# Kernel tuning notes

Measured on AMD Instinct MI355X. Metric: run time of the kernel, lower is better.

The kernel has to match this reference:

```python
import jax, jax.numpy as jnp
import numpy as np
import math

B, S, D, H = 4, 2048, 1024, 16
DK = D // H  # 64
THETA = 10000.0


def setup_inputs() -> dict:
    key = jax.random.key(0)
    ks = jax.random.split(key, 5)
    std = 0.02
    return {
        "x": jax.random.normal(ks[0], (B, S, D), dtype=jnp.float32),
        "Wq": jax.random.normal(ks[1], (D, D), dtype=jnp.float32) * std,
        "Wk": jax.random.normal(ks[2], (D, D), dtype=jnp.float32) * std,
        "Wv": jax.random.normal(ks[3], (D, D), dtype=jnp.float32) * std,
        "Wo": jax.random.normal(ks[4], (D, D), dtype=jnp.float32) * std / math.sqrt(2 * 12),
        "token_positions": jnp.arange(S, dtype=jnp.int32),
    }


def _rope(x, pos):
    # x: [B, H, S, DK]; pos: [S]. Interleaved-pair rotary embedding.
    inv_freq = THETA ** (-jnp.arange(0, DK, 2, dtype=jnp.float32) / DK)  # [DK/2]
    ang = pos.astype(jnp.float32)[:, None] * inv_freq[None, :]  # [S, DK/2]
    cos, sin = jnp.cos(ang), jnp.sin(ang)
    x1, x2 = x[..., 0::2], x[..., 1::2]  # [B, H, S, DK/2]
    r1 = x1 * cos - x2 * sin
    r2 = x1 * sin + x2 * cos
    return jnp.stack([r1, r2], axis=-1).reshape(x.shape)


def reference(x, Wq, Wk, Wv, Wo, token_positions):
    b, s, d = x.shape
    Q = x @ Wq
    K = x @ Wk
    V = x @ Wv
    # [B, S, D] -> [B, H, S, DK]
    def split(t):
        return t.reshape(b, s, H, DK).transpose(0, 2, 1, 3)
    Qh, Kh, Vh = split(Q), split(K), split(V)
    Qh = _rope(Qh, token_positions)
    Kh = _rope(Kh, token_positions)
    scores = jnp.einsum('bhqd,bhkd->bhqk', Qh, Kh) / math.sqrt(DK)
    causal = jnp.tril(jnp.ones((s, s), dtype=bool))
    scores = jnp.where(causal, scores, -jnp.inf)
    probs = jax.nn.softmax(scores, axis=-1)
    out = jnp.einsum('bhqk,bhkd->bhqd', probs, Vh)
    out = out.transpose(0, 2, 1, 3).reshape(b, s, d)
    return out @ Wo
```

## Files before the change

### kernel.cpp

```cpp
#include <hip/hip_runtime.h>
#include <hip/hip_bf16.h>

#define B_N 4
#define S_LEN 2048
#define D_MODEL 1024
#define N_HEAD 16
#define D_HEAD 64
#define M_ROWS (B_N * S_LEN)

typedef short bf16x8 __attribute__((ext_vector_type(8)));
typedef short bf16x4 __attribute__((ext_vector_type(4)));
typedef float f32x4 __attribute__((ext_vector_type(4)));

#if __has_builtin(__builtin_amdgcn_mfma_f32_16x16x16bf16_1k)
#define HAVE_MFMA16 1
#else
#define HAVE_MFMA16 0
#endif

__device__ __forceinline__ unsigned short f2bf(float f) {
  union { float f; unsigned int u; } v; v.f = f;
  unsigned int r = v.u + 0x7FFFu + ((v.u >> 16) & 1u);
  return (unsigned short)(r >> 16);
}
__device__ __forceinline__ float bf2f(unsigned short u) {
  union { unsigned int u; float f; } v; v.u = ((unsigned int)u) << 16;
  return v.f;
}
__device__ __forceinline__ unsigned int pkbf(float a, float b) {
  union { __hip_bfloat162 h; unsigned int u; } cv;
  cv.h = __float22bfloat162_rn(make_float2(a, b));
  return cv.u;
}
__device__ __forceinline__ bf16x8 ld8(const unsigned short* p) {
  return *reinterpret_cast<const bf16x8*>(p);
}
__device__ __forceinline__ bf16x4 ld4(const unsigned short* p) {
  return *reinterpret_cast<const bf16x4*>(p);
}
__device__ __forceinline__ void glds16(const unsigned short* g, unsigned short* l) {
  __builtin_amdgcn_global_load_lds(
      (const __attribute__((address_space(1))) unsigned int*)g,
      (__attribute__((address_space(3))) unsigned int*)l, 16, 0, 0);
}

__global__ __launch_bounds__(256) void rope_tab_k(const int* __restrict__ pos,
                                                  float2* __restrict__ tab) {
  const int idx = blockIdx.x * 256 + threadIdx.x;
  const int s = idx >> 5;
  const int i = idx & 31;
  const float inv = exp2f(-(float)i * 0.41524101186092029f);
  const float ang = (float)pos[s] * inv;
  tab[idx] = make_float2(cosf(ang), sinf(ang));
}

__global__ __launch_bounds__(256) void cast_k(const float* __restrict__ X,
                                              unsigned short* __restrict__ Y) {
  const size_t i = ((size_t)blockIdx.x * 256 + threadIdx.x) * 8;
  const float4 a = *reinterpret_cast<const float4*>(X + i);
  const float4 b = *reinterpret_cast<const float4*>(X + i + 4);
  union { unsigned int u[4]; uint4 v; } o;
  o.u[0] = pkbf(a.x, a.y); o.u[1] = pkbf(a.z, a.w);
  o.u[2] = pkbf(b.x, b.y); o.u[3] = pkbf(b.z, b.w);
  *reinterpret_cast<uint4*>(Y + i) = o.v;
}

__global__ __launch_bounds__(256) void wtrans_k(
    const float* __restrict__ W0, const float* __restrict__ W1,
    const float* __restrict__ W2, const float* __restrict__ W3,
    unsigned short* __restrict__ T0, unsigned short* __restrict__ T1,
    unsigned short* __restrict__ T2, unsigned short* __restrict__ T3) {
  const int z = blockIdx.z;
  const float* __restrict__ W = (z == 0) ? W0 : (z == 1) ? W1 : (z == 2) ? W2 : W3;
  unsigned short* __restrict__ T = (z == 0) ? T0 : (z == 1) ? T1 : (z == 2) ? T2 : T3;
  __shared__ __align__(16) unsigned short tile[64][72];
  const int kb = blockIdx.x * 64;
  const int nb = blockIdx.y * 64;
#pragma unroll
  for (int it = 0; it < 2; ++it) {
    const int chunk = it * 256 + threadIdx.x;
    const int r = chunk >> 3;
    const int c8 = (chunk & 7) * 8;
    const float* src = W + (size_t)(kb + r) * D_MODEL + nb + c8;
    const float4 a = *reinterpret_cast<const float4*>(src);
    const float4 b = *reinterpret_cast<const float4*>(src + 4);
    union { unsigned int u[4]; uint4 v; } o;
    o.u[0] = pkbf(a.x, a.y); o.u[1] = pkbf(a.z, a.w);
    o.u[2] = pkbf(b.x, b.y); o.u[3] = pkbf(b.z, b.w);
    *reinterpret_cast<uint4*>(&tile[r][c8]) = o.v;
  }
  __syncthreads();
#pragma unroll
  for (int it = 0; it < 2; ++it) {
    const int chunk = it * 256 + threadIdx.x;
    const int n = chunk >> 3;
    const int k8 = (chunk & 7) * 8;
    __align__(16) unsigned short vals[8];
#pragma unroll
    for (int j = 0; j < 8; ++j) vals[j] = tile[k8 + j][n];
    *reinterpret_cast<uint4*>(T + (size_t)(nb + n) * D_MODEL + kb + k8) =
        *reinterpret_cast<const uint4*>(vals);
  }
}

__global__ __launch_bounds__(512, 1) void gemm8_k(
    const unsigned short* __restrict__ A, const unsigned short* __restrict__ W,
    unsigned short* __restrict__ Qo, unsigned short* __restrict__ Ko,
    unsigned short* __restrict__ VTo, float* __restrict__ OF,
    const float2* __restrict__ tab) {
  __shared__ __align__(16) unsigned short smem[3][384 * 64];

  const int tid = threadIdx.x;
  const int lane = tid & 63;
  const int w = tid >> 6;
  const int l15 = lane & 15;
  const int l4 = lane >> 4;
  const int wm = w >> 2;
  const int wn = w & 3;

  const int row0 = blockIdx.x * 128;
  const int col0 = blockIdx.y * 256;

  const int srow = lane >> 3;
  const int schunk = (lane & 7) ^ srow;
  const unsigned short* gA = A + (size_t)(row0 + w * 8 + srow) * D_MODEL + schunk * 8;
  const unsigned short* gB = W + (size_t)(col0 + w * 8 + srow) * D_MODEL + schunk * 8;

  const int swz = l15 & 7;
  const int kc0 = ((l4) ^ swz) * 8;
  const int kc1 = ((l4 + 4) ^ swz) * 8;

  f32x4 acc[4][4];
  const f32x4 fz = {0.f, 0.f, 0.f, 0.f};
#pragma unroll
  for (int m = 0; m < 4; ++m)
#pragma unroll
    for (int n = 0; n < 4; ++n) acc[m][n] = fz;

#define G8_STAGE_A(SL, T)                                                      \
  do {                                                                         \
    unsigned short* sa_ = &smem[SL][(w * 8) * 64];                             \
    const unsigned short* g_ = gA + (size_t)(T) * 64;                          \
    glds16(g_, sa_);                                                           \
    glds16(g_ + 64 * D_MODEL, sa_ + 64 * 64);                                  \
  } while (0)

#define G8_STAGE_B(SL, T)                                                      \
  do {                                                                         \
    unsigned short* sb_ = &smem[SL][(128 + w * 8) * 64];                       \
    const unsigned short* g_ = gB + (size_t)(T) * 64;                          \
    glds16(g_, sb_);                                                           \
    glds16(g_ + 64 * D_MODEL, sb_ + 64 * 64);                                  \
    glds16(g_ + 128 * D_MODEL, sb_ + 128 * 64);                                \
    glds16(g_ + 192 * D_MODEL, sb_ + 192 * 64);                                \
  } while (0)

#define G8_PHASE(SL, KC, STG)                                                  \
  do {                                                                         \
    const unsigned short* As_ = &smem[SL][0];                                  \
    const unsigned short* Bs_ = &smem[SL][128 * 64];                           \
    bf16x8 af_[4], bf_[4];                                                     \
    _Pragma("unroll") for (int mi = 0; mi < 4; ++mi)                           \
      af_[mi] = ld8(As_ + (wm * 64 + mi * 16 + l15) * 64 + (KC));              \
    _Pragma("unroll") for (int ni = 0; ni < 4; ++ni)                           \
      bf_[ni] = ld8(Bs_ + (wn * 64 + ni * 16 + l15) * 64 + (KC));              \
    STG;                                                                       \
    __builtin_amdgcn_s_barrier();                                              \
    __builtin_amdgcn_s_setprio(1);                                             \
    _Pragma("unroll") for (int mi = 0; mi < 4; ++mi)                           \
      _Pragma("unroll") for (int ni = 0; ni < 4; ++ni)                         \
        acc[mi][ni] = __builtin_amdgcn_mfma_f32_16x16x32_bf16(                 \
            af_[mi], bf_[ni], acc[mi][ni], 0, 0, 0);                           \
    __builtin_amdgcn_s_setprio(0);                                             \
    __builtin_amdgcn_s_barrier();                                              \
  } while (0)

  G8_STAGE_A(0, 0); G8_STAGE_B(0, 0);
  G8_STAGE_A(1, 1); G8_STAGE_B(1, 1);

#pragma unroll
  for (int t = 0; t < 16; ++t) {
    const int sl = t % 3;
    const int sp = (t + 2) % 3;
    if (t < 15) {
      asm volatile("s_waitcnt vmcnt(6)" ::: "memory");
    } else {
      asm volatile("s_waitcnt vmcnt(0)" ::: "memory");
    }
    __builtin_amdgcn_s_barrier();
    if (t < 14) {
      G8_PHASE(sl, kc0, G8_STAGE_A(sp, (t + 2)));
      G8_PHASE(sl, kc1, G8_STAGE_B(sp, (t + 2)));
    } else {
      G8_PHASE(sl, kc0, ((void)0));
      G8_PHASE(sl, kc1, ((void)0));
    }
  }
#undef G8_STAGE_A
#undef G8_STAGE_B
#undef G8_PHASE

  if (OF) {
#pragma unroll
    for (int ni = 0; ni < 4; ++ni) {
      const int gcol = col0 + wn * 64 + ni * 16 + l15;
#pragma unroll
      for (int mi = 0; mi < 4; ++mi)
#pragma unroll
        for (int r = 0; r < 4; ++r)
          OF[(size_t)(row0 + wm * 64 + mi * 16 + l4 * 4 + r) * D_MODEL + gcol] =
              acc[mi][ni][r];
    }
    return;
  }

  unsigned short(*T)[68] =
      (unsigned short(*)[68])(&smem[0][0] + w * 4352);
  const int gcb = col0 + wn * 64;
  const bool isV = (gcb >= 2048);
  const int lr = lane >> 3;
  const int lc = lane & 7;

  if (!isV) {
#pragma unroll
    for (int mi = 0; mi < 4; ++mi)
#pragma unroll
      for (int n = 0; n < 4; ++n)
#pragma unroll
        for (int r = 0; r < 4; ++r)
          T[mi * 16 + l4 * 4 + r][n * 16 + l15] = f2bf(acc[mi][n][r]);
  } else {
#pragma unroll
    for (int mi = 0; mi < 4; ++mi)
#pragma unroll
      for (int n = 0; n < 4; ++n)
#pragma unroll
        for (int r = 0; r < 4; ++r)
          T[n * 16 + l15][mi * 16 + l4 * 4 + r] = f2bf(acc[mi][n][r]);
  }
  if (!isV) {
    const bool isQ = (gcb < 1024);
    unsigned short* O = isQ ? Qo : Ko;
    const float qs = isQ ? 0.18033688011112042f : 1.0f;
    const int cbase = gcb & 1023;
#pragma unroll
    for (int rg = 0; rg < 8; ++rg) {
      const int trow = rg * 8 + lr;
      const int grow = row0 + wm * 64 + trow;
      const int s = grow & (S_LEN - 1);
      const bf16x8 vv = ld8(&T[trow][lc * 8]);
      const float4 tA = *reinterpret_cast<const float4*>(&tab[s * 32 + lc * 4]);
      const float4 tB = *reinterpret_cast<const float4*>(&tab[s * 32 + lc * 4 + 2]);
      float x[8];
#pragma unroll
      for (int j = 0; j < 8; ++j) x[j] = bf2f((unsigned short)vv[j]);
      union { unsigned int u[4]; uint4 v; } o;
      o.u[0] = pkbf((x[0] * tA.x - x[1] * tA.y) * qs, (x[0] * tA.y + x[1] * tA.x) * qs);
      o.u[1] = pkbf((x[2] * tA.z - x[3] * tA.w) * qs, (x[2] * tA.w + x[3] * tA.z) * qs);
      o.u[2] = pkbf((x[4] * tB.x - x[5] * tB.y) * qs, (x[4] * tB.y + x[5] * tB.x) * qs);
      o.u[3] = pkbf((x[6] * tB.z - x[7] * tB.w) * qs, (x[6] * tB.w + x[7] * tB.z) * qs);
      *reinterpret_cast<uint4*>(O + (size_t)grow * D_MODEL + cbase + lc * 8) = o.v;
    }
  } else {
    const int vc0 = gcb - 2048;
    const int h = vc0 >> 6;
    const int bb = row0 >> 11;
    const int s0 = (row0 & (S_LEN - 1)) + wm * 64;
#pragma unroll
    for (int rg = 0; rg < 8; ++rg) {
      const int dk = rg * 8 + lr;
      const bf16x8 vv = ld8(&T[dk][lc * 8]);
      *reinterpret_cast<bf16x8*>(
          VTo + ((size_t)((bb << 4) + h) * 64 + dk) * S_LEN + s0 + lc * 8) = vv;
    }
  }
}

__global__ __launch_bounds__(512) void attn6_k(
    const unsigned short* __restrict__ Q, const unsigned short* __restrict__ K,
    const unsigned short* __restrict__ VT, unsigned short* __restrict__ O) {
  const int pair = blockIdx.x;
  const int h = blockIdx.y;
  const int b = blockIdx.z;
  const int tid = threadIdx.x;
  const int w = tid >> 6;
  const int lane = tid & 63;
  const int l15 = lane & 15;
  const int l4 = lane >> 4;

  __shared__ __align__(16) unsigned short Ks[64][72];
  __shared__ __align__(16) unsigned short Vs[64][72];
#if !HAVE_MFMA16
  __shared__ __align__(16) unsigned short Ps[8][16][72];
#endif

  const f32x4 fz = {0.f, 0.f, 0.f, 0.f};
  const unsigned short* kbase = K + (size_t)b * S_LEN * D_MODEL + h * D_HEAD;
  const unsigned short* vbase = VT + (size_t)((b << 4) + h) * 64 * S_LEN;

  const int rr = tid >> 3;
  const int c8 = (tid & 7) * 8;

  for (int half = 0; half < 2; ++half) {
    const int qt = half ? (15 - pair) : pair;
    const int qb = qt * 128;
    const int qw0 = qb + w * 16;

    bf16x8 qf[2];
#pragma unroll
    for (int kc = 0; kc < 2; ++kc)
      qf[kc] = ld8(Q + (size_t)(b * S_LEN + qw0 + l15) * D_MODEL +
                   h * D_HEAD + kc * 32 + l4 * 8);

    f32x4 o[4];
#pragma unroll
    for (int d = 0; d < 4; ++d) o[d] = fz;
    float lsum = 0.f;

    const int nkt = qb / 64 + 2;
    uint4 kreg = *reinterpret_cast<const uint4*>(kbase + (size_t)rr * D_MODEL + c8);
    uint4 vreg = *reinterpret_cast<const uint4*>(vbase + (size_t)rr * S_LEN + c8);

    for (int kt = 0; kt < nkt; ++kt) {
      const int kb0 = kt * 64;
      *reinterpret_cast<uint4*>(&Ks[rr][c8]) = kreg;
      *reinterpret_cast<uint4*>(&Vs[rr][c8]) = vreg;
      if (kt + 1 < nkt) {
        const int nb0 = kb0 + 64;
        kreg = *reinterpret_cast<const uint4*>(kbase + (size_t)(nb0 + rr) * D_MODEL + c8);
        vreg = *reinterpret_cast<const uint4*>(vbase + (size_t)rr * S_LEN + nb0 + c8);
      }
      __syncthreads();

      if (kb0 <= qw0 + 15) {
        f32x4 s[4];
#pragma unroll
        for (int n = 0; n < 4; ++n) {
          const bf16x8 kf0 = ld8(&Ks[n * 16 + l15][l4 * 8]);
          const bf16x8 kf1 = ld8(&Ks[n * 16 + l15][32 + l4 * 8]);
          f32x4 a0 = __builtin_amdgcn_mfma_f32_16x16x32_bf16(kf0, qf[0], fz, 0, 0, 0);
          s[n] = __builtin_amdgcn_mfma_f32_16x16x32_bf16(kf1, qf[1], a0, 0, 0, 0);
        }
        bf16x4 pf[4];
        const bool full = (kb0 + 63 <= qw0);
        const int q = qw0 + l15;
        float su = lsum;
#pragma unroll
        for (int n = 0; n < 4; ++n) {
          float e[4];
          if (full) {
#pragma unroll
            for (int r = 0; r < 4; ++r) e[r] = exp2f(s[n][r]);
          } else {
#pragma unroll
            for (int r = 0; r < 4; ++r) {
              const int key = kb0 + n * 16 + l4 * 4 + r;
              const float v = exp2f(s[n][r]);
              e[r] = (key <= q) ? v : 0.f;
            }
          }
          su += (e[0] + e[1]) + (e[2] + e[3]);
          union { unsigned int u[2]; bf16x4 v; } pk;
          pk.u[0] = pkbf(e[0], e[1]);
          pk.u[1] = pkbf(e[2], e[3]);
          pf[n] = pk.v;
        }
        lsum = su;

#if HAVE_MFMA16
#pragma unroll
        for (int d = 0; d < 4; ++d) {
          bf16x4 vfc[4];
#pragma unroll
          for (int c = 0; c < 4; ++c) vfc[c] = ld4(&Vs[d * 16 + l15][c * 16 + l4 * 4]);
#pragma unroll
          for (int c = 0; c < 4; ++c)
            o[d] = __builtin_amdgcn_mfma_f32_16x16x16bf16_1k(vfc[c], pf[c], o[d], 0, 0, 0);
        }
#else
#pragma unroll
        for (int n = 0; n < 4; ++n)
          *reinterpret_cast<bf16x4*>(&Ps[w][l15][n * 16 + l4 * 4]) = pf[n];
        bf16x8 pfr[2];
#pragma unroll
        for (int kc = 0; kc < 2; ++kc)
          pfr[kc] = ld8(&Ps[w][l15][kc * 32 + l4 * 8]);
#pragma unroll
        for (int d = 0; d < 4; ++d) {
          const bf16x8 vf0 = ld8(&Vs[d * 16 + l15][l4 * 8]);
          const bf16x8 vf1 = ld8(&Vs[d * 16 + l15][32 + l4 * 8]);
          o[d] = __builtin_amdgcn_mfma_f32_16x16x32_bf16(vf0, pfr[0], o[d], 0, 0, 0);
          o[d] = __builtin_amdgcn_mfma_f32_16x16x32_bf16(vf1, pfr[1], o[d], 0, 0, 0);
        }
#endif
      }
      __syncthreads();
    }

    float s = lsum;
    s += __shfl_xor(s, 16);
    s += __shfl_xor(s, 32);
    const float li = 1.0f / s;
    unsigned short* op = O + (size_t)(b * S_LEN + qw0 + l15) * D_MODEL +
                         h * D_HEAD + l4 * 4;
#pragma unroll
    for (int d = 0; d < 4; ++d) {
      union { unsigned int u[2]; uint2 v; } ov;
      ov.u[0] = pkbf(o[d][0] * li, o[d][1] * li);
      ov.u[1] = pkbf(o[d][2] * li, o[d][3] * li);
      *reinterpret_cast<uint2*>(op + d * 16) = ov.v;
    }
  }
}

extern "C" void kernel_launch(void* const* d_in, const int* in_sizes, int n_in,
                              void* d_out, int out_size, void* d_ws, size_t ws_size,
                              hipStream_t stream) {
  const float* x  = (const float*)d_in[0];
  const float* Wq = (const float*)d_in[1];
  const float* Wk = (const float*)d_in[2];
  const float* Wv = (const float*)d_in[3];
  const float* Wo = (const float*)d_in[4];
  const int* pos  = (const int*)d_in[5];
  float* out = (float*)d_out;

  char* ws = (char*)d_ws;
  const size_t big = (size_t)M_ROWS * D_MODEL * 2;
  const size_t wsz = (size_t)D_MODEL * D_MODEL * 2;
  unsigned short* xb  = (unsigned short*)(ws + 0 * big);
  unsigned short* Qb  = (unsigned short*)(ws + 1 * big);
  unsigned short* Kb  = (unsigned short*)(ws + 2 * big);
  unsigned short* VT  = (unsigned short*)(ws + 3 * big);
  unsigned short* Wqkvt = (unsigned short*)(ws + 4 * big);
  unsigned short* Wot   = (unsigned short*)(ws + 4 * big + 3 * wsz);
  float2* tab = (float2*)d_out;

  rope_tab_k<<<dim3(S_LEN * 32 / 256), 256, 0, stream>>>(pos, tab);
  cast_k<<<dim3(M_ROWS * D_MODEL / 2048), 256, 0, stream>>>(x, xb);
  wtrans_k<<<dim3(16, 16, 4), 256, 0, stream>>>(
      Wq, Wk, Wv, Wo, Wqkvt, Wqkvt + (size_t)D_MODEL * D_MODEL,
      Wqkvt + 2 * (size_t)D_MODEL * D_MODEL, Wot);
  gemm8_k<<<dim3(M_ROWS / 128, 3 * D_MODEL / 256), 512, 0, stream>>>(
      xb, Wqkvt, Qb, Kb, VT, nullptr, tab);
  attn6_k<<<dim3(8, N_HEAD, B_N), 512, 0, stream>>>(Qb, Kb, VT, Qb);
  gemm8_k<<<dim3(M_ROWS / 128, D_MODEL / 256), 512, 0, stream>>>(
      Qb, Wot, nullptr, nullptr, nullptr, out, nullptr);
}
```

Baseline: 254.2 us.

## Halve GEMM K-tile to 32 and allow two blocks per CU

The projection GEMM's shared-memory K tile drops from 64 to 32 columns, cutting the triple-buffered LDS footprint in half. Launch bounds change from one to two blocks per CU, so two 512-thread blocks can be resident at once. The pipeline becomes 32 single-phase iterations with a simpler 2-bit XOR swizzle and one fewer barrier per step. The cost is twice as many loop iterations and barriers per unit of work, and register pressure may tighten under the new occupancy target.

```diff
diff --git a/kernel.cpp b/kernel.cpp
--- a/kernel.cpp
+++ b/kernel.cpp
@@ -103,12 +103,12 @@
   }
 }
 
-__global__ __launch_bounds__(512, 1) void gemm8_k(
+__global__ __launch_bounds__(512, 2) void gemm8_k(
     const unsigned short* __restrict__ A, const unsigned short* __restrict__ W,
     unsigned short* __restrict__ Qo, unsigned short* __restrict__ Ko,
     unsigned short* __restrict__ VTo, float* __restrict__ OF,
     const float2* __restrict__ tab) {
-  __shared__ __align__(16) unsigned short smem[3][384 * 64];
+  __shared__ __align__(16) unsigned short smem[3][384 * 32];
 
   const int tid = threadIdx.x;
   const int lane = tid & 63;
@@ -121,14 +121,12 @@
   const int row0 = blockIdx.x * 128;
   const int col0 = blockIdx.y * 256;
 
-  const int srow = lane >> 3;
-  const int schunk = (lane & 7) ^ srow;
-  const unsigned short* gA = A + (size_t)(row0 + w * 8 + srow) * D_MODEL + schunk * 8;
-  const unsigned short* gB = W + (size_t)(col0 + w * 8 + srow) * D_MODEL + schunk * 8;
-
-  const int swz = l15 & 7;
-  const int kc0 = ((l4) ^ swz) * 8;
-  const int kc1 = ((l4 + 4) ^ swz) * 8;
+  const int srow4 = lane >> 2;
+  const int schunk = (lane & 3) ^ (srow4 & 3);
+  const unsigned short* gA = A + (size_t)(row0 + w * 16 + srow4) * D_MODEL + schunk * 8;
+  const unsigned short* gB = W + (size_t)(col0 + w * 16 + srow4) * D_MODEL + schunk * 8;
+
+  const int kc = (l4 ^ (l15 & 3)) * 8;
 
   f32x4 acc[4][4];
   const f32x4 fz = {0.f, 0.f, 0.f, 0.f};
@@ -137,33 +135,23 @@
 #pragma unroll
     for (int n = 0; n < 4; ++n) acc[m][n] = fz;
 
-#define G8_STAGE_A(SL, T)                                                      \
+#define G8_STAGE(SL, T)                                                        \
   do {                                                                         \
-    unsigned short* sa_ = &smem[SL][(w * 8) * 64];                             \
-    const unsigned short* g_ = gA + (size_t)(T) * 64;                          \
-    glds16(g_, sa_);                                                           \
-    glds16(g_ + 64 * D_MODEL, sa_ + 64 * 64);                                  \
+    glds16(gA + (size_t)(T) * 32, &smem[SL][w * 512]);                         \
+    glds16(gB + (size_t)(T) * 32, &smem[SL][4096 + w * 512]);                  \
+    glds16(gB + (size_t)128 * D_MODEL + (size_t)(T) * 32,                      \
+           &smem[SL][8192 + w * 512]);                                         \
   } while (0)
 
-#define G8_STAGE_B(SL, T)                                                      \
-  do {                                                                         \
-    unsigned short* sb_ = &smem[SL][(128 + w * 8) * 64];                       \
-    const unsigned short* g_ = gB + (size_t)(T) * 64;                          \
-    glds16(g_, sb_);                                                           \
-    glds16(g_ + 64 * D_MODEL, sb_ + 64 * 64);                                  \
-    glds16(g_ + 128 * D_MODEL, sb_ + 128 * 64);                                \
-    glds16(g_ + 192 * D_MODEL, sb_ + 192 * 64);                                \
-  } while (0)
-
-#define G8_PHASE(SL, KC, STG)                                                  \
+#define G8_PHASE(SL, STG)                                                      \
   do {                                                                         \
     const unsigned short* As_ = &smem[SL][0];                                  \
-    const unsigned short* Bs_ = &smem[SL][128 * 64];                           \
+    const unsigned short* Bs_ = &smem[SL][4096];                               \
     bf16x8 af_[4], bf_[4];                                                     \
     _Pragma("unroll") for (int mi = 0; mi < 4; ++mi)                           \
-      af_[mi] = ld8(As_ + (wm * 64 + mi * 16 + l15) * 64 + (KC));              \
+      af_[mi] = ld8(As_ + (wm * 64 + mi * 16 + l15) * 32 + kc);                \
     _Pragma("unroll") for (int ni = 0; ni < 4; ++ni)                           \
-      bf_[ni] = ld8(Bs_ + (wn * 64 + ni * 16 + l15) * 64 + (KC));              \
+      bf_[ni] = ld8(Bs_ + (wn * 64 + ni * 16 + l15) * 32 + kc);                \
     STG;                                                                       \
     __builtin_amdgcn_s_barrier();                                              \
     __builtin_amdgcn_s_setprio(1);                                             \
@@ -172,32 +160,26 @@
         acc[mi][ni] = __builtin_amdgcn_mfma_f32_16x16x32_bf16(                 \
             af_[mi], bf_[ni], acc[mi][ni], 0, 0, 0);                           \
     __builtin_amdgcn_s_setprio(0);                                             \
-    __builtin_amdgcn_s_barrier();                                              \
   } while (0)
 
-  G8_STAGE_A(0, 0); G8_STAGE_B(0, 0);
-  G8_STAGE_A(1, 1); G8_STAGE_B(1, 1);
-
-#pragma unroll
-  for (int t = 0; t < 16; ++t) {
+  G8_STAGE(0, 0);
+  G8_STAGE(1, 1);
+  asm volatile("s_waitcnt vmcnt(3)" ::: "memory");
+  __builtin_amdgcn_s_barrier();
+
+  for (int t = 0; t < 32; ++t) {
     const int sl = t % 3;
     const int sp = (t + 2) % 3;
-    if (t < 15) {
-      asm volatile("s_waitcnt vmcnt(6)" ::: "memory");
+    if (t < 30) {
+      G8_PHASE(sl, G8_STAGE(sp, (t + 2)));
+      asm volatile("s_waitcnt vmcnt(3)" ::: "memory");
     } else {
-      asm volatile("s_waitcnt vmcnt(0)" ::: "memory");
+      G8_PHASE(sl, ((void)0));
+      if (t == 30) asm volatile("s_waitcnt vmcnt(0)" ::: "memory");
     }
     __builtin_amdgcn_s_barrier();
-    if (t < 14) {
-      G8_PHASE(sl, kc0, G8_STAGE_A(sp, (t + 2)));
-      G8_PHASE(sl, kc1, G8_STAGE_B(sp, (t + 2)));
-    } else {
-      G8_PHASE(sl, kc0, ((void)0));
-      G8_PHASE(sl, kc1, ((void)0));
-    }
-  }
-#undef G8_STAGE_A
-#undef G8_STAGE_B
+  }
+#undef G8_STAGE
 #undef G8_PHASE
 
   if (OF) {
```

Result: slower. 275.2 us (+8.2%).
